# Kernel optimization log

Hardware: AMD Instinct MI355X
Metric: run time of the kernel (lower is better)

The kernel has to match this reference:

```python
import jax, jax.numpy as jnp
import numpy as np

ROUTING_ITERS = 3

def _squash(s, axis=-1):
    # v = s * ||s||^2 / (1 + ||s||^2) / ||s||
    n2 = jnp.sum(s * s, axis=axis, keepdims=True)
    return s * n2 / (1.0 + n2) / jnp.sqrt(n2 + 1e-8)

def setup_inputs() -> dict:
    key = jax.random.key(0)
    k1, k2, k3 = jax.random.split(key, 3)
    B, R, C, O, I = 256, 1152, 10, 16, 8
    x = jax.random.normal(k1, (B, R, I), dtype=jnp.float32)
    W = jax.random.normal(k2, (R, C, O, I), dtype=jnp.float32) * 0.05
    bias = jax.random.normal(k3, (C, O), dtype=jnp.float32) * 0.05
    return {"x": x, "W": W, "bias": bias}

def reference(x, W, bias):
    # x: [B,R,I], W: [R,C,O,I], bias: [C,O]
    B = x.shape[0]
    R, C, O, I = W.shape
    # u_hat[b,r,c,o] = W[r,c,o,:] . x[b,r,:]   (torch: matmul(W, x) over broadcast batch)
    u_hat = jnp.einsum('rcoi,bri->brco', W, x)  # [B,R,C,O]
    b_ij = jnp.zeros((R, C), dtype=x.dtype)
    v = None
    for it in range(ROUTING_ITERS):
        c_ij = jax.nn.softmax(b_ij, axis=1)  # softmax over capsules (dim=2 in torch layout)
        s = jnp.einsum('rc,brco->bco', c_ij, u_hat) + bias  # [B,C,O]
        v = _squash(s, axis=-1)  # squash over out_channels (dim=-2 of [B,1,C,O,1])
        if it < ROUTING_ITERS - 1:
            # agreement: u_hat^T v, then mean over batch (keepdim collapses to shared logits)
            agree = jnp.einsum('brco,bco->brc', u_hat, v).mean(axis=0)  # [R,C]
            b_ij = b_ij + agree
    # torch returns v_j.squeeze(1): [B, C, O, 1]
    return v[..., None]
```

## Files before the change

### kernel.cpp

```cpp
#include <hip/hip_runtime.h>

#define CB 256
#define CR 1152
#define CC 10
#define CO 16
#define CI 8
#define CK (CR*CI)
#define NCO (CC*CO)

typedef __bf16 bf16_t;
typedef __attribute__((ext_vector_type(8))) __bf16 bf16x8;
typedef __attribute__((ext_vector_type(4))) float f32x4;

__device__ __forceinline__ unsigned short bfbits(float f) {
  union { __bf16 h; unsigned short u; } u; u.h = (bf16_t)f; return u.u;
}

template<int MODE, bool LAST>
__global__ __launch_bounds__(512) void k_s(const float* __restrict__ x,
                                           const float* __restrict__ W,
                                           const float* __restrict__ bias,
                                           const float* __restrict__ cwT,
                                           bf16_t* __restrict__ vTb,
                                           float* __restrict__ out) {
  const int blk = blockIdx.x;
  const int xcd = blk & 7, j = blk >> 3;
  const int bt = (xcd & 3) * 4 + (j & 3);
  const int c  = (xcd >> 2) * 5 + (j >> 2);
  const int t = threadIdx.x;
  const int w = t >> 6, lane = t & 63;
  const int mrow = lane & 15, kg = lane >> 4;
  const int b0 = bt * 16;

  __shared__ float cwS[CR];
  __shared__ float Ls[8][64][4];
  if (MODE == 1) {
    if (t < CR / 4) ((float4*)cwS)[t] = ((const float4*)(cwT + (size_t)c * CR))[t];
    __syncthreads();
  }

  const int r0w = w * 144;
  const float4* ax = (const float4*)(x + (size_t)(b0 + mrow) * CK + (size_t)w * 1152) + kg * 2;

  f32x4 acc = {0.f, 0.f, 0.f, 0.f};
  #pragma unroll 4
  for (int s = 0; s < 36; ++s) {
    const float4 a0 = ax[s * 8], a1 = ax[s * 8 + 1];
    const int r = r0w + s * 4 + kg;
    const float4* wp = (const float4*)(W + (((size_t)r * CC + c) * CO + mrow) * CI);
    const float4 w0 = wp[0], w1 = wp[1];
    bf16x8 af, bf;
    af[0] = (bf16_t)a0.x; af[1] = (bf16_t)a0.y; af[2] = (bf16_t)a0.z; af[3] = (bf16_t)a0.w;
    af[4] = (bf16_t)a1.x; af[5] = (bf16_t)a1.y; af[6] = (bf16_t)a1.z; af[7] = (bf16_t)a1.w;
    if (MODE == 1) {
      const float cw = cwS[r];
      bf[0] = (bf16_t)(w0.x * cw); bf[1] = (bf16_t)(w0.y * cw);
      bf[2] = (bf16_t)(w0.z * cw); bf[3] = (bf16_t)(w0.w * cw);
      bf[4] = (bf16_t)(w1.x * cw); bf[5] = (bf16_t)(w1.y * cw);
      bf[6] = (bf16_t)(w1.z * cw); bf[7] = (bf16_t)(w1.w * cw);
    } else {
      bf[0] = (bf16_t)w0.x; bf[1] = (bf16_t)w0.y; bf[2] = (bf16_t)w0.z; bf[3] = (bf16_t)w0.w;
      bf[4] = (bf16_t)w1.x; bf[5] = (bf16_t)w1.y; bf[6] = (bf16_t)w1.z; bf[7] = (bf16_t)w1.w;
    }
    acc = __builtin_amdgcn_mfma_f32_16x16x32_bf16(af, bf, acc, 0, 0, 0);
  }

  #pragma unroll
  for (int reg = 0; reg < 4; ++reg) Ls[w][lane][reg] = acc[reg];
  __syncthreads();

  if (t < 256) {
    const int row = t >> 4, col = t & 15;
    const int l = ((row >> 2) << 4) | col, reg = row & 3;
    float s = 0.f;
    #pragma unroll
    for (int q = 0; q < 8; ++q) s += Ls[q][l][reg];
    if (MODE == 0) s *= 0.1f;
    s += bias[c * CO + col];
    float n2 = s * s;
    #pragma unroll
    for (int m = 1; m < 16; m <<= 1) n2 += __shfl_xor(n2, m);
    const float vv = s * n2 / (1.f + n2) * rsqrtf(n2 + 1e-8f);
    if (LAST) out[(size_t)(b0 + row) * NCO + c * CO + col] = vv;
    else      vTb[(size_t)(c * CO + col) * CB + b0 + row] = (bf16_t)vv;
  }
}

template<bool FIRST>
__global__ __launch_bounds__(512) void k_asc(const float* __restrict__ x,
                                             const float* __restrict__ W,
                                             const bf16_t* __restrict__ vTb,
                                             float* __restrict__ b_ij,
                                             float* __restrict__ cwT) {
  const int r0 = blockIdx.x * 8;
  const int t = threadIdx.x;
  const int h = t >> 8;
  const int th = t & 255;
  const int w = th >> 6, lane = th & 63;
  const int mrow = lane & 15, kg = lane >> 4;

  __shared__ __align__(16) unsigned short vL[NCO][CB + 8];
  __shared__ __align__(16) unsigned short xTl[64][CB + 8];
  __shared__ float agrL[8][CC];
  __shared__ float cwL[8][CC];

  #pragma unroll
  for (int q = 0; q < 10; ++q) {
    const int idx = q * 512 + t;
    const int co = idx >> 5, bs = idx & 31;
    const bf16x8 v = ((const bf16x8*)vTb)[idx];
    *(bf16x8*)&vL[co][bs * 8] = v;
  }
  #pragma unroll
  for (int chunk = 0; chunk < 16; ++chunk) {
    const int b = chunk * 16 + (t >> 5);
    const int ri = (t & 31) * 2;
    const float2 v = *(const float2*)(x + (size_t)b * CK + r0 * 8 + ri);
    xTl[ri][b] = bfbits(v.x);
    xTl[ri + 1][b] = bfbits(v.y);
  }
  __syncthreads();

  bf16x8 a[8];
  #pragma unroll
  for (int s = 0; s < 8; ++s)
    a[s] = *(const bf16x8*)&xTl[w * 16 + mrow][s * 32 + kg * 8];

  const int o = lane & 15, g = lane >> 4;
  #pragma unroll
  for (int cc = 0; cc < 5; ++cc) {
    const int c = h * 5 + cc;
    f32x4 acc = {0.f, 0.f, 0.f, 0.f};
    #pragma unroll
    for (int s = 0; s < 8; ++s) {
      const bf16x8 bv = *(const bf16x8*)&vL[c * CO + mrow][s * 32 + kg * 8];
      acc = __builtin_amdgcn_mfma_f32_16x16x32_bf16(a[s], bv, acc, 0, 0, 0);
    }
    float p = 0.f;
    #pragma unroll
    for (int reg = 0; reg < 4; ++reg) {
      const int m = g * 4 + reg, rl = m >> 3, i = m & 7;
      p += acc[reg] * W[(((size_t)(r0 + w * 2 + rl) * CC + c) * CO + o) * CI + i];
    }
    #pragma unroll
    for (int msk = 1; msk < 32; msk <<= 1) p += __shfl_xor(p, msk);
    if ((lane & 31) == 0) agrL[w * 2 + (lane >> 5)][c] = p * (1.0f / CB);
  }
  __syncthreads();

  if (t < 8) {
    const int r = r0 + t;
    float nb[CC];
    float mx = -1e30f;
    #pragma unroll
    for (int c = 0; c < CC; ++c) {
      nb[c] = (FIRST ? 0.f : b_ij[r * CC + c]) + agrL[t][c];
      mx = fmaxf(mx, nb[c]);
    }
    float sum = 0.f;
    #pragma unroll
    for (int c = 0; c < CC; ++c) {
      b_ij[r * CC + c] = nb[c];
      const float e = __expf(nb[c] - mx);
      cwL[t][c] = e;
      sum += e;
    }
    const float inv = 1.f / sum;
    #pragma unroll
    for (int c = 0; c < CC; ++c) cwT[(size_t)c * CR + r] = cwL[t][c] * inv;
  }
}

extern "C" void kernel_launch(void* const* d_in, const int* in_sizes, int n_in,
                              void* d_out, int out_size, void* d_ws, size_t ws_size,
                              hipStream_t stream) {
  const float* x    = (const float*)d_in[0];
  const float* W    = (const float*)d_in[1];
  const float* bias = (const float*)d_in[2];
  float* out = (float*)d_out;

  bf16_t* vTb  = (bf16_t*)d_ws;
  float*  b_ij = (float*)(vTb + (size_t)NCO * CB);
  float*  cwT  = b_ij + (size_t)CR * CC;

  k_s<0, false><<<160, 512, 0, stream>>>(x, W, bias, cwT, vTb, out);
  k_asc<true><<<144, 512, 0, stream>>>(x, W, vTb, b_ij, cwT);

  k_s<1, false><<<160, 512, 0, stream>>>(x, W, bias, cwT, vTb, out);
  k_asc<false><<<144, 512, 0, stream>>>(x, W, vTb, b_ij, cwT);

  k_s<1, true><<<160, 512, 0, stream>>>(x, W, bias, cwT, vTb, out);
}
```

Measured before the change: 103.9 us.

## Cache bf16 x and pre-scaled bf16 W so later s-passes stream half-size operands

The first s-pass now also writes bf16 copies of x and a transposed bf16 W into workspace. The agreement kernel writes W pre-multiplied by the softmax coupling weights (Wts) instead of a cwT array. Later s-passes then run pure bf16 MFMA loads with no per-element conversion or scaling, using 1024-thread blocks and two accumulators. This roughly halves the operand bytes the later passes read and removes conversion ALU work, at the cost of extra global writes in the first pass and the agreement kernel.

Result: faster. 97.49 us (-6.1%).

```diff
diff --git a/kernel.cpp b/kernel.cpp
--- a/kernel.cpp
+++ b/kernel.cpp
@@ -16,66 +16,95 @@
   union { __bf16 h; unsigned short u; } u; u.h = (bf16_t)f; return u.u;
 }
 
-template<int MODE, bool LAST>
-__global__ __launch_bounds__(512) void k_s(const float* __restrict__ x,
-                                           const float* __restrict__ W,
-                                           const float* __restrict__ bias,
-                                           const float* __restrict__ cwT,
-                                           bf16_t* __restrict__ vTb,
-                                           float* __restrict__ out) {
+__global__ __launch_bounds__(1024) void k_s0(const float* __restrict__ x,
+                                             const float* __restrict__ W,
+                                             const float* __restrict__ bias,
+                                             bf16_t* __restrict__ xb,
+                                             bf16_t* __restrict__ Wt,
+                                             bf16_t* __restrict__ vTb) {
   const int blk = blockIdx.x;
   const int xcd = blk & 7, j = blk >> 3;
-  const int bt = (xcd & 3) * 4 + (j & 3);
-  const int c  = (xcd >> 2) * 5 + (j >> 2);
+  const int bt = xcd * 2 + (j & 1);
+  const int c = j >> 1;
   const int t = threadIdx.x;
   const int w = t >> 6, lane = t & 63;
   const int mrow = lane & 15, kg = lane >> 4;
   const int b0 = bt * 16;
 
-  __shared__ float cwS[CR];
-  __shared__ float Ls[8][64][4];
-  if (MODE == 1) {
-    if (t < CR / 4) ((float4*)cwS)[t] = ((const float4*)(cwT + (size_t)c * CR))[t];
-    __syncthreads();
-  }
-
-  const int r0w = w * 144;
-  const float4* ax = (const float4*)(x + (size_t)(b0 + mrow) * CK + (size_t)w * 1152) + kg * 2;
-
+  const float* ax = x + (size_t)(b0 + mrow) * CK + w * 576;
   f32x4 acc = {0.f, 0.f, 0.f, 0.f};
-  #pragma unroll 4
-  for (int s = 0; s < 36; ++s) {
-    const float4 a0 = ax[s * 8], a1 = ax[s * 8 + 1];
-    const int r = r0w + s * 4 + kg;
-    const float4* wp = (const float4*)(W + (((size_t)r * CC + c) * CO + mrow) * CI);
-    const float4 w0 = wp[0], w1 = wp[1];
+  #pragma unroll 3
+  for (int s = 0; s < 18; ++s) {
+    const int koff = s * 32 + kg * 8;
+    const float4 a0 = *(const float4*)(ax + koff);
+    const float4 a1 = *(const float4*)(ax + koff + 4);
     bf16x8 af, bf;
     af[0] = (bf16_t)a0.x; af[1] = (bf16_t)a0.y; af[2] = (bf16_t)a0.z; af[3] = (bf16_t)a0.w;
     af[4] = (bf16_t)a1.x; af[5] = (bf16_t)a1.y; af[6] = (bf16_t)a1.z; af[7] = (bf16_t)a1.w;
-    if (MODE == 1) {
-      const float cw = cwS[r];
-      bf[0] = (bf16_t)(w0.x * cw); bf[1] = (bf16_t)(w0.y * cw);
-      bf[2] = (bf16_t)(w0.z * cw); bf[3] = (bf16_t)(w0.w * cw);
-      bf[4] = (bf16_t)(w1.x * cw); bf[5] = (bf16_t)(w1.y * cw);
-      bf[6] = (bf16_t)(w1.z * cw); bf[7] = (bf16_t)(w1.w * cw);
-    } else {
-      bf[0] = (bf16_t)w0.x; bf[1] = (bf16_t)w0.y; bf[2] = (bf16_t)w0.z; bf[3] = (bf16_t)w0.w;
-      bf[4] = (bf16_t)w1.x; bf[5] = (bf16_t)w1.y; bf[6] = (bf16_t)w1.z; bf[7] = (bf16_t)w1.w;
-    }
+    const int r = w * 72 + s * 4 + kg;
+    const float4* wp = (const float4*)(W + (((size_t)r * CC + c) * CO + mrow) * CI);
+    const float4 w0 = wp[0], w1 = wp[1];
+    bf[0] = (bf16_t)w0.x; bf[1] = (bf16_t)w0.y; bf[2] = (bf16_t)w0.z; bf[3] = (bf16_t)w0.w;
+    bf[4] = (bf16_t)w1.x; bf[5] = (bf16_t)w1.y; bf[6] = (bf16_t)w1.z; bf[7] = (bf16_t)w1.w;
+    if (c == 0)  *(bf16x8*)(xb + (size_t)(b0 + mrow) * CK + w * 576 + koff) = af;
+    if (bt == 0) *(bf16x8*)(Wt + ((size_t)c * CO + mrow) * CK + w * 576 + koff) = bf;
     acc = __builtin_amdgcn_mfma_f32_16x16x32_bf16(af, bf, acc, 0, 0, 0);
   }
 
+  __shared__ float Ls[16][64][4];
   #pragma unroll
   for (int reg = 0; reg < 4; ++reg) Ls[w][lane][reg] = acc[reg];
   __syncthreads();
-
   if (t < 256) {
     const int row = t >> 4, col = t & 15;
     const int l = ((row >> 2) << 4) | col, reg = row & 3;
     float s = 0.f;
     #pragma unroll
-    for (int q = 0; q < 8; ++q) s += Ls[q][l][reg];
-    if (MODE == 0) s *= 0.1f;
+    for (int q = 0; q < 16; ++q) s += Ls[q][l][reg];
+    s = s * 0.1f + bias[c * CO + col];
+    float n2 = s * s;
+    #pragma unroll
+    for (int m = 1; m < 16; m <<= 1) n2 += __shfl_xor(n2, m);
+    const float vv = s * n2 / (1.f + n2) * rsqrtf(n2 + 1e-8f);
+    vTb[(size_t)(c * CO + col) * CB + b0 + row] = (bf16_t)vv;
+  }
+}
+
+template<bool LAST>
+__global__ __launch_bounds__(1024) void k_s(const bf16_t* __restrict__ xb,
+                                            const bf16_t* __restrict__ Wts,
+                                            const float* __restrict__ bias,
+                                            bf16_t* __restrict__ vTb,
+                                            float* __restrict__ out) {
+  const int blk = blockIdx.x;
+  const int xcd = blk & 7, j = blk >> 3;
+  const int bt = xcd * 2 + (j & 1);
+  const int c = j >> 1;
+  const int t = threadIdx.x;
+  const int w = t >> 6, lane = t & 63;
+  const int mrow = lane & 15, kg = lane >> 4;
+  const int b0 = bt * 16;
+
+  const bf16x8* ap = (const bf16x8*)(xb + (size_t)(b0 + mrow) * CK + w * 576) + kg;
+  const bf16x8* bp = (const bf16x8*)(Wts + ((size_t)c * CO + mrow) * CK + w * 576) + kg;
+  f32x4 acc0 = {0.f, 0.f, 0.f, 0.f}, acc1 = {0.f, 0.f, 0.f, 0.f};
+  #pragma unroll
+  for (int s = 0; s < 18; s += 2) {
+    acc0 = __builtin_amdgcn_mfma_f32_16x16x32_bf16(ap[s * 4], bp[s * 4], acc0, 0, 0, 0);
+    acc1 = __builtin_amdgcn_mfma_f32_16x16x32_bf16(ap[(s + 1) * 4], bp[(s + 1) * 4], acc1, 0, 0, 0);
+  }
+  const f32x4 acc = acc0 + acc1;
+
+  __shared__ float Ls[16][64][4];
+  #pragma unroll
+  for (int reg = 0; reg < 4; ++reg) Ls[w][lane][reg] = acc[reg];
+  __syncthreads();
+  if (t < 256) {
+    const int row = t >> 4, col = t & 15;
+    const int l = ((row >> 2) << 4) | col, reg = row & 3;
+    float s = 0.f;
+    #pragma unroll
+    for (int q = 0; q < 16; ++q) s += Ls[q][l][reg];
     s += bias[c * CO + col];
     float n2 = s * s;
     #pragma unroll
@@ -90,8 +119,9 @@
 __global__ __launch_bounds__(512) void k_asc(const float* __restrict__ x,
                                              const float* __restrict__ W,
                                              const bf16_t* __restrict__ vTb,
+                                             const bf16_t* __restrict__ Wt,
                                              float* __restrict__ b_ij,
-                                             float* __restrict__ cwT) {
+                                             bf16_t* __restrict__ Wts) {
   const int r0 = blockIdx.x * 8;
   const int t = threadIdx.x;
   const int h = t >> 8;
@@ -167,7 +197,23 @@
     }
     const float inv = 1.f / sum;
     #pragma unroll
-    for (int c = 0; c < CC; ++c) cwT[(size_t)c * CR + r] = cwL[t][c] * inv;
+    for (int c = 0; c < CC; ++c) cwL[t][c] *= inv;
+  }
+  __syncthreads();
+
+  #pragma unroll
+  for (int q = 0; q < 3; ++q) {
+    const int slot = q * 512 + t;
+    if (slot < 1280) {
+      const int co = slot >> 3, rl = slot & 7;
+      const float cw = cwL[rl][co >> 4];
+      const size_t off = (size_t)co * CK + (r0 + rl) * 8;
+      const bf16x8 wv = *(const bf16x8*)(Wt + off);
+      bf16x8 ov;
+      #pragma unroll
+      for (int jj = 0; jj < 8; ++jj) ov[jj] = (bf16_t)((float)wv[jj] * cw);
+      *(bf16x8*)(Wts + off) = ov;
+    }
   }
 }
 
@@ -179,15 +225,17 @@
   const float* bias = (const float*)d_in[2];
   float* out = (float*)d_out;
 
-  bf16_t* vTb  = (bf16_t*)d_ws;
+  bf16_t* xb  = (bf16_t*)d_ws;
+  bf16_t* Wt  = xb  + (size_t)CB * CK;
+  bf16_t* Wts = Wt  + (size_t)NCO * CK;
+  bf16_t* vTb = Wts + (size_t)NCO * CK;
   float*  b_ij = (float*)(vTb + (size_t)NCO * CB);
-  float*  cwT  = b_ij + (size_t)CR * CC;
-
-  k_s<0, false><<<160, 512, 0, stream>>>(x, W, bias, cwT, vTb, out);
-  k_asc<true><<<144, 512, 0, stream>>>(x, W, vTb, b_ij, cwT);
-
-  k_s<1, false><<<160, 512, 0, stream>>>(x, W, bias, cwT, vTb, out);
-  k_asc<false><<<144, 512, 0, stream>>>(x, W, vTb, b_ij, cwT);
-
-  k_s<1, true><<<160, 512, 0, stream>>>(x, W, bias, cwT, vTb, out);
-}
+
+  k_s0<<<160, 1024, 0, stream>>>(x, W, bias, xb, Wt, vTb);
+  k_asc<true><<<144, 512, 0, stream>>>(x, W, vTb, Wt, b_ij, Wts);
+
+  k_s<false><<<160, 1024, 0, stream>>>(xb, Wts, bias, vTb, out);
+  k_asc<false><<<144, 512, 0, stream>>>(x, W, vTb, Wt, b_ij, Wts);
+
+  k_s<true><<<160, 1024, 0, stream>>>(xb, Wts, bias, vTb, out);
+}
```
